# Performance work log

Hardware: AMD Instinct MI355X
Metric: run time of the kernel (lower is better)

The kernel has to match this reference:

```python
import jax, jax.numpy as jnp
import numpy as np
import math

HEAD_DIM = 64           # d_model // n_heads // 2
N_HEADS = 8
LAMBDA_INIT = 0.8 - 0.6 * math.exp(-0.3 * 6)  # depth=6
EPS = 1e-5


def setup_inputs() -> dict:
    key = jax.random.key(0)
    ks = jax.random.split(key, 8)
    B, T, S = 2, 2048, 2048
    return {
        "queries": jax.random.normal(ks[0], (B, 2 * N_HEADS, T, HEAD_DIM), jnp.float32),
        "keys": jax.random.normal(ks[1], (B, 2 * N_HEADS, S, HEAD_DIM), jnp.float32),
        "values": jax.random.normal(ks[2], (B, N_HEADS, S, 2 * HEAD_DIM), jnp.float32),
        "lambda_q1": 0.02 * jax.random.normal(ks[3], (HEAD_DIM,), jnp.float32),
        "lambda_k1": 0.02 * jax.random.normal(ks[4], (HEAD_DIM,), jnp.float32),
        "lambda_q2": 0.02 * jax.random.normal(ks[5], (HEAD_DIM,), jnp.float32),
        "lambda_k2": 0.02 * jax.random.normal(ks[6], (HEAD_DIM,), jnp.float32),
        "subln_weight": jnp.ones((2 * HEAD_DIM,), jnp.float32),
        "tgt_len": 2048,
        "src_len": 2048,
        "attn_mask": jnp.zeros((1,), jnp.bool_),
    }


def reference(queries, keys, values, lambda_q1, lambda_k1, lambda_q2, lambda_k2,
              subln_weight, tgt_len, src_len, attn_mask):
    B = queries.shape[0]
    scaling = HEAD_DIM ** -0.5
    q = queries * scaling
    # [B, 2H, T, S]
    attn_w = jnp.einsum('bhtd,bhsd->bhts', q, keys)
    attn_w = jax.nn.softmax(attn_w.astype(jnp.float32), axis=-1).astype(queries.dtype)
    lam1 = jnp.exp(jnp.sum(lambda_q1 * lambda_k1))
    lam2 = jnp.exp(jnp.sum(lambda_q2 * lambda_k2))
    lam_full = lam1 - lam2 + LAMBDA_INIT
    attn_w = attn_w.reshape(B, N_HEADS, 2, tgt_len, src_len)
    attn_w = attn_w[:, :, 0] - lam_full * attn_w[:, :, 1]   # [B, H, T, S]
    attn = jnp.einsum('bhts,bhse->bhte', attn_w, values)    # [B, H, T, 2*HEAD_DIM]
    # RMSNorm over last dim
    normed = attn * jax.lax.rsqrt(jnp.mean(jnp.square(attn.astype(jnp.float32)), axis=-1, keepdims=True) + EPS).astype(attn.dtype)
    normed = normed * subln_weight
    out = normed * (1.0 - LAMBDA_INIT)
    out = out.transpose(0, 2, 1, 3).reshape(B, tgt_len, N_HEADS * 2 * HEAD_DIM)
    return out
```

## Files before the change

kernel.cpp:

```cpp
#include <hip/hip_runtime.h>
#include <math.h>


#define NT    2048
#define D     64
#define DV    128
#define TQ    64
#define TS    32
#define NROUND (NT / (2 * TS))

#define LAMBDA_INIT 0.70082066706704814f
#define OUT_SCALE   0.29917933293295186f
#define QSCALE      0.18033688011112042f

typedef __attribute__((ext_vector_type(8)))  short    short8;
typedef __attribute__((ext_vector_type(4)))  short    short4v;
typedef __attribute__((ext_vector_type(8)))  _Float16 half8;
typedef __attribute__((ext_vector_type(2)))  __fp16   fp16x2;
typedef __attribute__((ext_vector_type(4)))  float    f32x4;
typedef unsigned short u16;
typedef unsigned int   u32;

#define MFMAH(a, b, c)  __builtin_amdgcn_mfma_f32_16x16x32_f16(a, b, c, 0, 0, 0)
#define MFMA16(a, b, c) __builtin_amdgcn_mfma_f32_16x16x32_bf16(a, b, c, 0, 0, 0)

#if __has_builtin(__builtin_amdgcn_exp2f)
#define EXP2F(x) __builtin_amdgcn_exp2f(x)
#else
#define EXP2F(x) exp2f(x)
#endif

union Hu { half8 v; _Float16 e[8]; u16 s[8]; short8 sv; };

__device__ __forceinline__ u16 f2h(float x) {
    Hu u; u.e[0] = (_Float16)x; return u.s[0];
}

__device__ __forceinline__ void glds16(const u16* g, const u16* l) {
    __builtin_amdgcn_global_load_lds(
        (const __attribute__((address_space(1))) void*)g,
        (__attribute__((address_space(3))) void*)l, 16, 0, 0);
}

__global__ __launch_bounds__(256) void prep_kv(
    const float* __restrict__ Kg, const float* __restrict__ Vg,
    const float* __restrict__ lq1, const float* __restrict__ lk1,
    const float* __restrict__ lq2, const float* __restrict__ lk2,
    u16* __restrict__ Kf, u16* __restrict__ Vf, float* __restrict__ lamw)
{
    __shared__ u16 th[64 * 136];
    const int bid = blockIdx.x;
    const int t   = threadIdx.x;
    if (bid < 2048) {
        const int idx = (bid * 256 + t) * 8;
        const float4 a = *(const float4*)(Kg + idx);
        const float4 b = *(const float4*)(Kg + idx + 4);
        Hu H;
        H.e[0] = (_Float16)a.x; H.e[1] = (_Float16)a.y;
        H.e[2] = (_Float16)a.z; H.e[3] = (_Float16)a.w;
        H.e[4] = (_Float16)b.x; H.e[5] = (_Float16)b.y;
        H.e[6] = (_Float16)b.z; H.e[7] = (_Float16)b.w;
        *(short8*)(Kf + idx) = H.sv;
        return;
    }
    if (bid == 2048) {
        if (t == 0) {
            float t1 = 0.f, t2 = 0.f;
            for (int i = 0; i < D; ++i) {
                t1 = fmaf(lq1[i], lk1[i], t1);
                t2 = fmaf(lq2[i], lk2[i], t2);
            }
            lamw[0] = __expf(t1) - __expf(t2) + LAMBDA_INIT;
        }
        return;
    }
    const int i  = bid - 2049;
    const int bh = i >> 5;
    const int eb = (i >> 4) & 1;
    const int sb = i & 15;
    const size_t vbase = (size_t)bh * NT * DV + (size_t)sb * 128 * DV + eb * 64;
    {
        const int r0 = t >> 4;
        const int c4 = (t & 15) * 4;
        #pragma unroll
        for (int rr = 0; rr < 8; ++rr) {
            const int row = r0 + rr * 16;
            const float4 x = *(const float4*)(Vg + vbase + (size_t)row * DV + c4);
            th[(c4 + 0) * 136 + row] = f2h(x.x);
            th[(c4 + 1) * 136 + row] = f2h(x.y);
            th[(c4 + 2) * 136 + row] = f2h(x.z);
            th[(c4 + 3) * 136 + row] = f2h(x.w);
        }
    }
    __syncthreads();
    const int e  = t >> 2;
    const int g  = t & 3;
    const size_t orow = ((size_t)bh * DV + eb * 64 + e) * NT + sb * 128;
    #pragma unroll
    for (int c = 0; c < 4; ++c) {
        Hu o;
        #pragma unroll
        for (int j = 0; j < 8; ++j)
            o.s[j] = th[e * 136 + g * 32 + 4 * c + (j & 3) + 16 * (j >> 2)];
        *(short8*)(Vf + orow + g * 32 + c * 8) = o.sv;
    }
}

struct SmemF {
    union {
        short8 c[4096];
        struct {
            float epi[2][32][132];
            float lbuf[2][2][2][32];
        } e;
    };
};

__global__ __launch_bounds__(512, 4) void diffattn_mfma12(
    const float* __restrict__ Qg,
    const u16* __restrict__ Kf, const u16* __restrict__ Vf,
    const float* __restrict__ lamw,
    const float* __restrict__ Wg, float* __restrict__ Outg)
{
    __shared__ SmemF sm;

    const int tid    = threadIdx.x;
    const int wv     = tid >> 6;
    const int lane   = tid & 63;
    const int quad   = lane >> 4;
    const int lc     = lane & 15;
    const int stripe = wv & 1;
    const int hh     = (wv >> 1) & 1;
    const int ks     = wv >> 2;
    const int wig    = wv & 3;
    const int qt     = blockIdx.x;
    const int bh     = blockIdx.y;
    const int b      = bh >> 3, h = bh & 7;

    const int head2b = b * 16 + 2 * h;
    const int bh8    = b * 8 + h;
    const float lam  = lamw[0];

    half8 qf[2][2];
    {
        const size_t qhead = (size_t)(head2b + hh) * NT * D;
        #pragma unroll
        for (int nq = 0; nq < 2; ++nq) {
            const int row = qt * TQ + stripe * 32 + nq * 16 + lc;
            #pragma unroll
            for (int k0 = 0; k0 < 2; ++k0) {
                const int d0 = k0 * 32 + quad * 8;
                const float4 x = *(const float4*)(Qg + qhead + (size_t)row * D + d0);
                const float4 y = *(const float4*)(Qg + qhead + (size_t)row * D + d0 + 4);
                Hu q;
                q.e[0] = (_Float16)(x.x * QSCALE); q.e[1] = (_Float16)(x.y * QSCALE);
                q.e[2] = (_Float16)(x.z * QSCALE); q.e[3] = (_Float16)(x.w * QSCALE);
                q.e[4] = (_Float16)(y.x * QSCALE); q.e[5] = (_Float16)(y.y * QSCALE);
                q.e[6] = (_Float16)(y.z * QSCALE); q.e[7] = (_Float16)(y.w * QSCALE);
                qf[nq][k0] = q.v;
            }
        }
    }

    f32x4 O_[2][8];
    #pragma unroll
    for (int nq = 0; nq < 2; ++nq)
        #pragma unroll
        for (int nt = 0; nt < 8; ++nt) O_[nq][nt] = (f32x4){0.f, 0.f, 0.f, 0.f};
    float lac[2] = {0.f, 0.f};

    u32 kSrc[2], vSrc[2];
    u32 kLds[2], vLds[2];
    #pragma unroll
    for (int t = 0; t < 2; ++t) {
        const int p   = (wig * 2 + t) * 64 + lane;
        const int hhs = p >> 8;
        const int n   = (p >> 3) & 31;
        const int db  = (p & 7) ^ (n & 7);
        kSrc[t] = (u32)(((head2b + hhs) * NT + n) * D + db * 8);
        kLds[t] = (u32)((ks * 512 + (wig * 2 + t) * 64) * 16);
        const int e = p >> 2;
        const int u = (p & 3) ^ ((e >> 1) & 3);
        vSrc[t] = (u32)((bh8 * DV + e) * NT + u * 8);
        vLds[t] = (u32)((1024 + ks * 512 + (wig * 2 + t) * 64) * 16);
    }
    const u16* ldsu = (const u16*)&sm.c[0];

    #pragma unroll
    for (int t = 0; t < 2; ++t) {
        glds16(Kf + kSrc[t] + (u32)ks * (TS * D), ldsu + (kLds[t] >> 1));
        glds16(Vf + vSrc[t] + (u32)ks * TS,       ldsu + (vLds[t] >> 1));
    }
    __syncthreads();

    u32 kOff[2][2];
    #pragma unroll
    for (int k0 = 0; k0 < 2; ++k0)
        #pragma unroll
        for (int mt = 0; mt < 2; ++mt)
            kOff[k0][mt] = (u32)((ks * 512 + hh * 256 + (mt * 16 + lc) * 8 +
                                  ((4 * k0 + quad) ^ (lc & 7))) * 8);
    u32 vOff[8];
    {
        const int swzv = quad ^ ((lc >> 1) & 3);
        #pragma unroll
        for (int nt = 0; nt < 8; ++nt)
            vOff[nt] = (u32)((1024 + ks * 512 + (nt * 16 + lc) * 4 + swzv) * 8);
    }

    const fp16x2 ones = {(__fp16)1.f, (__fp16)1.f};

    for (int r = 0; r < NROUND; ++r) {
        const u32 bo = ((u32)(r & 1)) << 14;

        if (r < NROUND - 1) {
            const u32 tn = (u32)(2 * (r + 1) + ks);
            const u32 ab = ((u32)((r + 1) & 1)) << 14;
            #pragma unroll
            for (int t = 0; t < 2; ++t) {
                glds16(Kf + kSrc[t] + tn * (TS * D), ldsu + ab + (kLds[t] >> 1));
                glds16(Vf + vSrc[t] + tn * TS,       ldsu + ab + (vLds[t] >> 1));
            }
        }

        f32x4 sf[2][2];
        #pragma unroll
        for (int mt = 0; mt < 2; ++mt)
            #pragma unroll
            for (int nq = 0; nq < 2; ++nq) sf[mt][nq] = (f32x4){0.f, 0.f, 0.f, 0.f};
        #pragma unroll
        for (int k0 = 0; k0 < 2; ++k0) {
            #pragma unroll
            for (int mt = 0; mt < 2; ++mt) {
                const half8 kfr = *(const half8*)(ldsu + bo + kOff[k0][mt]);
                #pragma unroll
                for (int nq = 0; nq < 2; ++nq)
                    sf[mt][nq] = MFMAH(kfr, qf[nq][k0], sf[mt][nq]);
            }
        }

        half8 a8[2];
        #pragma unroll
        for (int nq = 0; nq < 2; ++nq) {
            union { half8 v; fp16x2 h[4]; } a;
            float ls = lac[nq];
            #pragma unroll
            for (int mt = 0; mt < 2; ++mt)
                #pragma unroll
                for (int ip = 0; ip < 2; ++ip) {
                    const float p0 = EXP2F(sf[mt][nq][2 * ip]);
                    const float p1 = EXP2F(sf[mt][nq][2 * ip + 1]);
                    const fp16x2 h2 = __builtin_amdgcn_cvt_pkrtz(p0, p1);
                    a.h[mt * 2 + ip] = h2;
                    ls = __builtin_amdgcn_fdot2(h2, ones, ls, false);
                }
            lac[nq] = ls;
            a8[nq] = a.v;
        }

        #pragma unroll
        for (int nt = 0; nt < 8; ++nt) {
            const half8 vfr = *(const half8*)(ldsu + bo + vOff[nt]);
            #pragma unroll
            for (int nq = 0; nq < 2; ++nq)
                O_[nq][nt] = MFMAH(a8[nq], vfr, O_[nq][nt]);
        }

        __syncthreads();
    }

    {
        float s0 = lac[0], s1 = lac[1];
        s0 += __shfl_xor(s0, 16); s0 += __shfl_xor(s0, 32);
        s1 += __shfl_xor(s1, 16); s1 += __shfl_xor(s1, 32);
        if (quad == 0) {
            sm.e.lbuf[hh][ks][stripe][lc]      = s0;
            sm.e.lbuf[hh][ks][stripe][16 + lc] = s1;
        }
    }
    __syncthreads();
    float coef[2][4];
    #pragma unroll
    for (int nq = 0; nq < 2; ++nq)
        #pragma unroll
        for (int i = 0; i < 4; ++i) {
            const int row = nq * 16 + quad * 4 + i;
            const float lt = sm.e.lbuf[hh][0][stripe][row] +
                             sm.e.lbuf[hh][1][stripe][row];
            coef[nq][i] = (hh == 0) ? (1.f / lt) : (-lam / lt);
        }
    __syncthreads();
    const int pid = hh * 2 + ks;
    #pragma unroll
    for (int p = 0; p < 4; ++p) {
        if (pid == p) {
            #pragma unroll
            for (int nq = 0; nq < 2; ++nq)
                #pragma unroll
                for (int i = 0; i < 4; ++i) {
                    const int row = nq * 16 + quad * 4 + i;
                    #pragma unroll
                    for (int nt = 0; nt < 8; ++nt) {
                        const int col = nt * 16 + lc;
                        const float v = O_[nq][nt][i] * coef[nq][i];
                        if (p == 0) sm.e.epi[stripe][row][col] = v;
                        else        sm.e.epi[stripe][row][col] += v;
                    }
                }
        }
        __syncthreads();
    }
    {
        const int r0 = wv * 8 + (lane >> 3);
        const int st = r0 >> 5, ri = r0 & 31;
        const int e0 = (lane & 7) * 16;
        float x[16];
        float ssq = 0.f;
        #pragma unroll
        for (int m = 0; m < 16; m += 4) {
            const float4 t4 = *(const float4*)&sm.e.epi[st][ri][e0 + m];
            x[m] = t4.x; x[m + 1] = t4.y; x[m + 2] = t4.z; x[m + 3] = t4.w;
            ssq += t4.x * t4.x + t4.y * t4.y + t4.z * t4.z + t4.w * t4.w;
        }
        ssq += __shfl_xor(ssq, 1);
        ssq += __shfl_xor(ssq, 2);
        ssq += __shfl_xor(ssq, 4);
        const float rsq = rsqrtf(ssq * (1.f / 128.f) + 1e-5f) * OUT_SCALE;
        const int rowg = qt * TQ + r0;
        const size_t base =
            ((size_t)b * NT + rowg) * (size_t)(8 * DV) + (size_t)h * DV;
        #pragma unroll
        for (int m = 0; m < 16; m += 4) {
            const float4 w4 = *(const float4*)(Wg + e0 + m);
            float4 o4;
            o4.x = x[m] * rsq * w4.x;
            o4.y = x[m + 1] * rsq * w4.y;
            o4.z = x[m + 2] * rsq * w4.z;
            o4.w = x[m + 3] * rsq * w4.w;
            *(float4*)(Outg + base + e0 + m) = o4;
        }
    }
}

__device__ __forceinline__ unsigned short f2bf(float x) {
    unsigned u = __float_as_uint(x);
    return (unsigned short)((u + 0x7fffu + ((u >> 16) & 1u)) >> 16);
}
__device__ __forceinline__ float bf2f(unsigned short h) {
    return __uint_as_float(((unsigned)h) << 16);
}

struct SmemB {
    union {
        struct {
            short8 kh[2][264];
            short8 kl[2][264];
            short8 vh[516];
            short8 vl[516];
            unsigned short ph[2][2560];
            unsigned short pl[2][2560];
        } L;
        float epi[2][32][132];
    };
};

__global__ __launch_bounds__(256, 2) void diffattn_fb(
    const float* __restrict__ Qg, const float* __restrict__ Kg,
    const float* __restrict__ Vg,
    const float* __restrict__ lq1, const float* __restrict__ lk1,
    const float* __restrict__ lq2, const float* __restrict__ lk2,
    const float* __restrict__ Wg, float* __restrict__ Outg)
{
    __shared__ SmemB sm;
    const int tid = threadIdx.x;
    const int wv = tid >> 6, lane = tid & 63;
    const int quad = lane >> 4, lc = lane & 15;
    const int stripe = wv & 1, hh = wv >> 1;
    const int qt = blockIdx.x, bh = blockIdx.y;
    const int b = bh >> 3, h = bh & 7;
    const size_t koff0 = ((size_t)(b * 16 + 2 * h)) * NT * D;
    const size_t voff  = ((size_t)(b * 8 + h)) * NT * DV;
    float t1 = 0.f, t2 = 0.f;
    for (int i = 0; i < D; ++i) {
        t1 = fmaf(lq1[i], lk1[i], t1);
        t2 = fmaf(lq2[i], lk2[i], t2);
    }
    const float lam = __expf(t1) - __expf(t2) + LAMBDA_INIT;
    short8 qfh[2][2], qfl[2][2];
    {
        const size_t qhead = ((size_t)(b * 16 + 2 * h + hh)) * NT * D;
        #pragma unroll
        for (int mt = 0; mt < 2; ++mt)
            #pragma unroll
            for (int k0 = 0; k0 < 2; ++k0) {
                const int row = qt * TQ + stripe * 32 + mt * 16 + lc;
                const int d0  = k0 * 32 + quad * 8;
                const float4 x = *(const float4*)(Qg + qhead + (size_t)row * D + d0);
                const float4 y = *(const float4*)(Qg + qhead + (size_t)row * D + d0 + 4);
                float f[8] = {x.x, x.y, x.z, x.w, y.x, y.y, y.z, y.w};
                #pragma unroll
                for (int j = 0; j < 8; ++j) {
                    const float v = f[j] * 0.125f;
                    const unsigned short hi = f2bf(v);
                    qfh[mt][k0][j] = (short)hi;
                    qfl[mt][k0][j] = (short)f2bf(v - bf2f(hi));
                }
            }
    }
    f32x4 O_[2][8];
    #pragma unroll
    for (int mt = 0; mt < 2; ++mt)
        #pragma unroll
        for (int nt = 0; nt < 8; ++nt) O_[mt][nt] = (f32x4){0.f, 0.f, 0.f, 0.f};
    float m_[2][4], l_[2][4], a_[2][4];
    #pragma unroll
    for (int mt = 0; mt < 2; ++mt)
        #pragma unroll
        for (int i = 0; i < 4; ++i) { m_[mt][i] = -1e30f; l_[mt][i] = 0.f; }
    const int s_hh = tid >> 7;
    const int s_n  = (tid >> 2) & 31;
    const int s_d0 = (tid & 3) * 16;
    const int s_e0 = tid & 31;
    const int s_s0 = ((tid >> 5) & 7) * 4;
    const int s_sb = s_s0 >> 3;
    const int s_hs = (s_s0 & 4) ? 1 : 0;
    for (int kt = 0; kt < NT / TS; ++kt) {
        const int kb = kt * TS;
        __syncthreads();
        {
            const float* kp = Kg + koff0 + (size_t)s_hh * NT * D +
                              (size_t)(kb + s_n) * D + s_d0;
            const float4 x0 = ((const float4*)kp)[0];
            const float4 x1 = ((const float4*)kp)[1];
            const float4 x2 = ((const float4*)kp)[2];
            const float4 x3 = ((const float4*)kp)[3];
            float f[16] = {x0.x, x0.y, x0.z, x0.w, x1.x, x1.y, x1.z, x1.w,
                           x2.x, x2.y, x2.z, x2.w, x3.x, x3.y, x3.z, x3.w};
            short8 c0h, c0l, c1h, c1l;
            #pragma unroll
            for (int j = 0; j < 8; ++j) {
                unsigned short hi = f2bf(f[j]);
                c0h[j] = (short)hi; c0l[j] = (short)f2bf(f[j] - bf2f(hi));
                hi = f2bf(f[8 + j]);
                c1h[j] = (short)hi; c1l[j] = (short)f2bf(f[8 + j] - bf2f(hi));
            }
            const int db0 = s_d0 >> 3;
            sm.L.kh[s_hh][db0 * 33 + s_n]       = c0h;
            sm.L.kl[s_hh][db0 * 33 + s_n]       = c0l;
            sm.L.kh[s_hh][(db0 + 1) * 33 + s_n] = c1h;
            sm.L.kl[s_hh][(db0 + 1) * 33 + s_n] = c1l;
        }
        {
            #pragma unroll
            for (int j = 0; j < 4; ++j) {
                const int e = s_e0 + 32 * j;
                float f[4];
                #pragma unroll
                for (int i = 0; i < 4; ++i)
                    f[i] = Vg[voff + (size_t)(kb + s_s0 + i) * DV + e];
                short4v hi4, lo4;
                #pragma unroll
                for (int i = 0; i < 4; ++i) {
                    const unsigned short hi = f2bf(f[i]);
                    hi4[i] = (short)hi;
                    lo4[i] = (short)f2bf(f[i] - bf2f(hi));
                }
                ((short4v*)&sm.L.vh[s_sb * 129 + e])[s_hs] = hi4;
                ((short4v*)&sm.L.vl[s_sb * 129 + e])[s_hs] = lo4;
            }
        }
        __syncthreads();
        f32x4 s_f[2][2];
        #pragma unroll
        for (int mt = 0; mt < 2; ++mt)
            #pragma unroll
            for (int nt = 0; nt < 2; ++nt) s_f[mt][nt] = (f32x4){0.f, 0.f, 0.f, 0.f};
        #pragma unroll
        for (int k0 = 0; k0 < 2; ++k0)
            #pragma unroll
            for (int nt = 0; nt < 2; ++nt) {
                const short8 kh = sm.L.kh[hh][(4 * k0 + quad) * 33 + nt * 16 + lc];
                const short8 kl = sm.L.kl[hh][(4 * k0 + quad) * 33 + nt * 16 + lc];
                #pragma unroll
                for (int mt = 0; mt < 2; ++mt) {
                    s_f[mt][nt] = MFMA16(qfh[mt][k0], kh, s_f[mt][nt]);
                    s_f[mt][nt] = MFMA16(qfl[mt][k0], kh, s_f[mt][nt]);
                    s_f[mt][nt] = MFMA16(qfh[mt][k0], kl, s_f[mt][nt]);
                }
            }
        #pragma unroll
        for (int mt = 0; mt < 2; ++mt)
            #pragma unroll
            for (int i = 0; i < 4; ++i) {
                const float v0 = s_f[mt][0][i], v1 = s_f[mt][1][i];
                float mx = fmaxf(v0, v1);
                mx = fmaxf(mx, __shfl_xor(mx, 1));
                mx = fmaxf(mx, __shfl_xor(mx, 2));
                mx = fmaxf(mx, __shfl_xor(mx, 4));
                mx = fmaxf(mx, __shfl_xor(mx, 8));
                const float mn = fmaxf(m_[mt][i], mx);
                const float al = __expf(m_[mt][i] - mn);
                const float p0 = __expf(v0 - mn);
                const float p1 = __expf(v1 - mn);
                float rs = p0 + p1;
                rs += __shfl_xor(rs, 1);
                rs += __shfl_xor(rs, 2);
                rs += __shfl_xor(rs, 4);
                rs += __shfl_xor(rs, 8);
                l_[mt][i] = l_[mt][i] * al + rs;
                m_[mt][i] = mn;
                a_[mt][i] = al;
                const int r = stripe * 32 + mt * 16 + quad * 4 + i;
                const unsigned short h0 = f2bf(p0);
                sm.L.ph[hh][r * 40 + lc]      = h0;
                sm.L.pl[hh][r * 40 + lc]      = f2bf(p0 - bf2f(h0));
                const unsigned short h1 = f2bf(p1);
                sm.L.ph[hh][r * 40 + 16 + lc] = h1;
                sm.L.pl[hh][r * 40 + 16 + lc] = f2bf(p1 - bf2f(h1));
            }
        __syncthreads();
        #pragma unroll
        for (int mt = 0; mt < 2; ++mt)
            #pragma unroll
            for (int nt = 0; nt < 8; ++nt)
                #pragma unroll
                for (int i = 0; i < 4; ++i) O_[mt][nt][i] *= a_[mt][i];
        short8 pah[2], pal[2];
        #pragma unroll
        for (int mt = 0; mt < 2; ++mt) {
            const int r = stripe * 32 + mt * 16 + lc;
            pah[mt] = *(const short8*)&sm.L.ph[hh][r * 40 + quad * 8];
            pal[mt] = *(const short8*)&sm.L.pl[hh][r * 40 + quad * 8];
        }
        #pragma unroll
        for (int nt = 0; nt < 8; ++nt) {
            const short8 vh = sm.L.vh[quad * 129 + nt * 16 + lc];
            const short8 vl = sm.L.vl[quad * 129 + nt * 16 + lc];
            #pragma unroll
            for (int mt = 0; mt < 2; ++mt) {
                O_[mt][nt] = MFMA16(pah[mt], vh, O_[mt][nt]);
                O_[mt][nt] = MFMA16(pal[mt], vh, O_[mt][nt]);
                O_[mt][nt] = MFMA16(pah[mt], vl, O_[mt][nt]);
            }
        }
    }
    __syncthreads();
    if (hh == 1) {
        #pragma unroll
        for (int mt = 0; mt < 2; ++mt)
            #pragma unroll
            for (int i = 0; i < 4; ++i) {
                const float inv = lam / l_[mt][i];
                const int r = mt * 16 + quad * 4 + i;
                #pragma unroll
                for (int nt = 0; nt < 8; ++nt)
                    sm.epi[stripe][r][nt * 16 + lc] = O_[mt][nt][i] * inv;
            }
    }
    __syncthreads();
    if (hh == 0) {
        float wvv[8];
        #pragma unroll
        for (int nt = 0; nt < 8; ++nt) wvv[nt] = Wg[nt * 16 + lc];
        #pragma unroll
        for (int mt = 0; mt < 2; ++mt)
            #pragma unroll
            for (int i = 0; i < 4; ++i) {
                const float inv1 = 1.f / l_[mt][i];
                const int r = mt * 16 + quad * 4 + i;
                float od[8];
                float ss = 0.f;
                #pragma unroll
                for (int nt = 0; nt < 8; ++nt) {
                    od[nt] = O_[mt][nt][i] * inv1 - sm.epi[stripe][r][nt * 16 + lc];
                    ss = fmaf(od[nt], od[nt], ss);
                }
                ss += __shfl_xor(ss, 1);
                ss += __shfl_xor(ss, 2);
                ss += __shfl_xor(ss, 4);
                ss += __shfl_xor(ss, 8);
                const float rsq = rsqrtf(ss * (1.f / 128.f) + 1e-5f) * OUT_SCALE;
                const int rowg = qt * TQ + stripe * 32 + r;
                const size_t base =
                    ((size_t)b * NT + rowg) * (size_t)(8 * DV) + (size_t)h * DV;
                #pragma unroll
                for (int nt = 0; nt < 8; ++nt)
                    Outg[base + nt * 16 + lc] = od[nt] * rsq * wvv[nt];
            }
    }
}

extern "C" void kernel_launch(void* const* d_in, const int* in_sizes, int n_in,
                              void* d_out, int out_size, void* d_ws, size_t ws_size,
                              hipStream_t stream) {
    const float* Q   = (const float*)d_in[0];
    const float* K   = (const float*)d_in[1];
    const float* V   = (const float*)d_in[2];
    const float* lq1 = (const float*)d_in[3];
    const float* lk1 = (const float*)d_in[4];
    const float* lq2 = (const float*)d_in[5];
    const float* lk2 = (const float*)d_in[6];
    const float* W   = (const float*)d_in[7];
    float* Out = (float*)d_out;
    const size_t NEED = 2ull * 4194304ull * sizeof(u16) + 16;
    if (ws_size >= NEED) {
        u16*   Kf   = (u16*)d_ws;
        u16*   Vf   = Kf + 4194304;
        float* lamw = (float*)(Vf + 4194304);
        prep_kv<<<2561, 256, 0, stream>>>(K, V, lq1, lk1, lq2, lk2, Kf, Vf, lamw);
        diffattn_mfma12<<<dim3(NT / TQ, 16), 512, 0, stream>>>(
            Q, Kf, Vf, lamw, W, Out);
    } else {
        diffattn_fb<<<dim3(NT / TQ, 16), 256, 0, stream>>>(
            Q, K, V, lq1, lk1, lq2, lk2, W, Out);
    }
}
```

Before: 169.6 us.

## Add MFMA priority hints, split row-sum chains, use LDS atomics in epilogue

The score MFMAs are rewritten with hoisted K fragment loads and zero-initialized accumulators, and s_setprio is raised around the MFMA groups so waves doing matrix work get issue priority. The row-sum accumulation is split into two independent fdot2 chains to shorten the dependency chain. In the epilogue, four serialized passes with a barrier each are replaced by one plain store pass followed by a single pass of LDS atomicAdd, which removes barriers but adds contention from the atomics.

Result: slower. 226.4 us (+33.5%).

```diff
diff --git a/kernel.cpp b/kernel.cpp
--- a/kernel.cpp
+++ b/kernel.cpp
@@ -116,7 +116,7 @@
     };
 };
 
-__global__ __launch_bounds__(512, 4) void diffattn_mfma12(
+__global__ __launch_bounds__(512, 4) void diffattn_mfma16(
     const float* __restrict__ Qg,
     const u16* __restrict__ Kf, const u16* __restrict__ Vf,
     const float* __restrict__ lamw,
@@ -167,7 +167,8 @@
     for (int nq = 0; nq < 2; ++nq)
         #pragma unroll
         for (int nt = 0; nt < 8; ++nt) O_[nq][nt] = (f32x4){0.f, 0.f, 0.f, 0.f};
-    float lac[2] = {0.f, 0.f};
+    float lacA[2] = {0.f, 0.f};
+    float lacB[2] = {0.f, 0.f};
 
     u32 kSrc[2], vSrc[2];
     u32 kLds[2], vLds[2];
@@ -208,7 +209,7 @@
             vOff[nt] = (u32)((1024 + ks * 512 + (nt * 16 + lc) * 4 + swzv) * 8);
     }
 
-    const fp16x2 ones = {(__fp16)1.f, (__fp16)1.f};
+    const f32x4 z4 = {0.f, 0.f, 0.f, 0.f};
 
     for (int r = 0; r < NROUND; ++r) {
         const u32 bo = ((u32)(r & 1)) << 14;
@@ -224,26 +225,29 @@
         }
 
         f32x4 sf[2][2];
-        #pragma unroll
-        for (int mt = 0; mt < 2; ++mt)
-            #pragma unroll
-            for (int nq = 0; nq < 2; ++nq) sf[mt][nq] = (f32x4){0.f, 0.f, 0.f, 0.f};
-        #pragma unroll
-        for (int k0 = 0; k0 < 2; ++k0) {
-            #pragma unroll
-            for (int mt = 0; mt < 2; ++mt) {
-                const half8 kfr = *(const half8*)(ldsu + bo + kOff[k0][mt]);
-                #pragma unroll
-                for (int nq = 0; nq < 2; ++nq)
-                    sf[mt][nq] = MFMAH(kfr, qf[nq][k0], sf[mt][nq]);
-            }
+        {
+            const half8 k00 = *(const half8*)(ldsu + bo + kOff[0][0]);
+            const half8 k01 = *(const half8*)(ldsu + bo + kOff[0][1]);
+            const half8 k10 = *(const half8*)(ldsu + bo + kOff[1][0]);
+            const half8 k11 = *(const half8*)(ldsu + bo + kOff[1][1]);
+            __builtin_amdgcn_s_setprio(1);
+            sf[0][0] = MFMAH(k00, qf[0][0], z4);
+            sf[0][1] = MFMAH(k00, qf[1][0], z4);
+            sf[1][0] = MFMAH(k01, qf[0][0], z4);
+            sf[1][1] = MFMAH(k01, qf[1][0], z4);
+            sf[0][0] = MFMAH(k10, qf[0][1], sf[0][0]);
+            sf[0][1] = MFMAH(k10, qf[1][1], sf[0][1]);
+            sf[1][0] = MFMAH(k11, qf[0][1], sf[1][0]);
+            sf[1][1] = MFMAH(k11, qf[1][1], sf[1][1]);
+            __builtin_amdgcn_s_setprio(0);
         }
 
         half8 a8[2];
         #pragma unroll
         for (int nq = 0; nq < 2; ++nq) {
             union { half8 v; fp16x2 h[4]; } a;
-            float ls = lac[nq];
+            float lsA = lacA[nq], lsB = lacB[nq];
+            const fp16x2 ones = {(__fp16)1.f, (__fp16)1.f};
             #pragma unroll
             for (int mt = 0; mt < 2; ++mt)
                 #pragma unroll
@@ -252,25 +256,31 @@
                     const float p1 = EXP2F(sf[mt][nq][2 * ip + 1]);
                     const fp16x2 h2 = __builtin_amdgcn_cvt_pkrtz(p0, p1);
                     a.h[mt * 2 + ip] = h2;
-                    ls = __builtin_amdgcn_fdot2(h2, ones, ls, false);
+                    if (((mt * 2 + ip) & 1) == 0)
+                        lsA = __builtin_amdgcn_fdot2(h2, ones, lsA, false);
+                    else
+                        lsB = __builtin_amdgcn_fdot2(h2, ones, lsB, false);
                 }
-            lac[nq] = ls;
+            lacA[nq] = lsA; lacB[nq] = lsB;
             a8[nq] = a.v;
         }
 
         #pragma unroll
         for (int nt = 0; nt < 8; ++nt) {
             const half8 vfr = *(const half8*)(ldsu + bo + vOff[nt]);
+            __builtin_amdgcn_s_setprio(1);
             #pragma unroll
             for (int nq = 0; nq < 2; ++nq)
                 O_[nq][nt] = MFMAH(a8[nq], vfr, O_[nq][nt]);
+            __builtin_amdgcn_s_setprio(0);
         }
 
         __syncthreads();
     }
 
     {
-        float s0 = lac[0], s1 = lac[1];
+        float s0 = lacA[0] + lacB[0];
+        float s1 = lacA[1] + lacB[1];
         s0 += __shfl_xor(s0, 16); s0 += __shfl_xor(s0, 32);
         s1 += __shfl_xor(s1, 16); s1 += __shfl_xor(s1, 32);
         if (quad == 0) {
@@ -291,25 +301,32 @@
         }
     __syncthreads();
     const int pid = hh * 2 + ks;
-    #pragma unroll
-    for (int p = 0; p < 4; ++p) {
-        if (pid == p) {
-            #pragma unroll
-            for (int nq = 0; nq < 2; ++nq)
-                #pragma unroll
-                for (int i = 0; i < 4; ++i) {
-                    const int row = nq * 16 + quad * 4 + i;
-                    #pragma unroll
-                    for (int nt = 0; nt < 8; ++nt) {
-                        const int col = nt * 16 + lc;
-                        const float v = O_[nq][nt][i] * coef[nq][i];
-                        if (p == 0) sm.e.epi[stripe][row][col] = v;
-                        else        sm.e.epi[stripe][row][col] += v;
-                    }
-                }
-        }
-        __syncthreads();
-    }
+    if (pid == 0) {
+        #pragma unroll
+        for (int nq = 0; nq < 2; ++nq)
+            #pragma unroll
+            for (int i = 0; i < 4; ++i) {
+                const int row = nq * 16 + quad * 4 + i;
+                #pragma unroll
+                for (int nt = 0; nt < 8; ++nt)
+                    sm.e.epi[stripe][row][nt * 16 + lc] =
+                        O_[nq][nt][i] * coef[nq][i];
+            }
+    }
+    __syncthreads();
+    if (pid != 0) {
+        #pragma unroll
+        for (int nq = 0; nq < 2; ++nq)
+            #pragma unroll
+            for (int i = 0; i < 4; ++i) {
+                const int row = nq * 16 + quad * 4 + i;
+                #pragma unroll
+                for (int nt = 0; nt < 8; ++nt)
+                    atomicAdd(&sm.e.epi[stripe][row][nt * 16 + lc],
+                              O_[nq][nt][i] * coef[nq][i]);
+            }
+    }
+    __syncthreads();
     {
         const int r0 = wv * 8 + (lane >> 3);
         const int st = r0 >> 5, ri = r0 & 31;
@@ -608,7 +625,7 @@
         u16*   Vf   = Kf + 4194304;
         float* lamw = (float*)(Vf + 4194304);
         prep_kv<<<2561, 256, 0, stream>>>(K, V, lq1, lk1, lq2, lk2, Kf, Vf, lamw);
-        diffattn_mfma12<<<dim3(NT / TQ, 16), 512, 0, stream>>>(
+        diffattn_mfma16<<<dim3(NT / TQ, 16), 512, 0, stream>>>(
             Q, Kf, Vf, lamw, W, Out);
     } else {
         diffattn_fb<<<dim3(NT / TQ, 16), 256, 0, stream>>>(
```
